# Kernel optimization log

Measured on AMD Instinct MI355X. Metric: run time of the kernel, lower is better.

The kernel has to match this reference:

```python
import jax, jax.numpy as jnp
import numpy as np

L1, L2, L3, L4 = 0.01, 0.001, 0.1, 100.0
DROP_P = 0.3

def setup_inputs() -> dict:
    key = jax.random.key(0)
    ks = jax.random.split(key, 6)
    n, p, h, c = 262144, 256, 256, 10
    x = jax.random.normal(ks[0], (n, p), dtype=jnp.float32)
    y = jax.random.randint(ks[1], (n,), 0, c, dtype=jnp.int64)
    drop_u = jax.random.uniform(ks[2], (n, h), dtype=jnp.float32)
    b1 = jax.random.normal(ks[3], (p, h), dtype=jnp.float32) / p
    b2 = jax.random.normal(ks[4], (h, c), dtype=jnp.float32) / h
    w = jax.random.normal(ks[5], (n, 1), dtype=jnp.float32) / n + 1.0 / np.sqrt(n).astype(np.float32)
    return {"x": x, "y": y, "drop_u": drop_u, "b1": b1, "b2": b2, "w": w}

def reference(x, y, drop_u, b1, b2, w):
    n, p = x.shape
    # MLP: ReLU -> Dropout(0.3) (inverted dropout, deterministic mask from drop_u)
    hdn = jax.nn.relu(x @ b1)
    keep = (drop_u > DROP_P).astype(x.dtype) / (1.0 - DROP_P)
    logits = (hdn * keep) @ b2  # [n, 10]
    pred = jnp.argmax(logits, axis=1)
    weight = w * w  # [n, 1]
    # per-sample CE; torch broadcast ce[n] * weight[n,1] -> [n,n], summed == ce.sum()*weight.sum()
    ce = -jnp.take_along_axis(jax.nn.log_softmax(logits, axis=-1), y[:, None], axis=1)[:, 0]
    loss = ce.sum() * weight.sum()
    # balancing regularizer: x.T @ diag(weight) @ x computed as column-scale-then-GEMM
    col = x.T @ weight  # [p, 1]
    gram = x.T @ (weight * x)  # [p, p] == x.T @ diag(weight) @ x
    bm = (gram - col @ col.T) * (1.0 - jnp.eye(p, dtype=x.dtype))
    loss = loss + L1 * (jnp.abs(b1).sum() + jnp.abs(b2).sum())
    loss = loss + L2 * jnp.sum(bm * bm)
    loss = loss + L3 * jnp.sum(weight * weight)
    loss = loss + L4 * (weight.sum() - 1.0) ** 2
    acc = jnp.mean((pred == y).astype(jnp.float32))
    return (loss, acc)
```

## Files before the change

### kernel.cpp

```cpp
#include <hip/hip_runtime.h>
#include <hip/hip_bf16.h>
#include <math.h>

typedef __bf16 v8bf  __attribute__((ext_vector_type(8)));
typedef __bf16 v4bf  __attribute__((ext_vector_type(4)));
typedef float  v16f  __attribute__((ext_vector_type(16)));
typedef float  v4f   __attribute__((ext_vector_type(4)));
typedef float  f4v   __attribute__((ext_vector_type(4)));

#define N_ROWS    262144
#define OFF_COL   64
#define OFF_GRAM  1024
#define OFF_WT    66560
#define B1T_BYTE  1314816
#define B2T_BYTE  1445888
#define ZERO_BYTES 266240

extern "C" __global__ __launch_bounds__(256) void prep_k(
    const float* __restrict__ w, const float* __restrict__ b1,
    const float* __restrict__ b2, float* __restrict__ wsf) {
  float* weight = wsf + OFF_WT;
  __bf16* b1T = (__bf16*)((char*)wsf + B1T_BYTE);
  __bf16* b2T = (__bf16*)((char*)wsf + B2T_BYTE);
  int gid = blockIdx.x * 256 + threadIdx.x;
  float wi = w[gid];
  float wt = wi * wi;
  weight[gid] = wt;
  float s1 = wt, s2 = wt * wt, a1 = 0.f, a2 = 0.f;
  if (gid < 65536) {
    int h = gid >> 8, p = gid & 255;
    float v = b1[p * 256 + h];
    b1T[gid] = (__bf16)v;
    a1 = fabsf(v);
  }
  if (gid < 4096) {
    int c = gid >> 8, h = gid & 255;
    float v = (c < 10) ? b2[h * 10 + c] : 0.f;
    b2T[gid] = (__bf16)v;
    a2 = fabsf(v);
  }
  #pragma unroll
  for (int off = 32; off > 0; off >>= 1) {
    s1 += __shfl_down(s1, off);
    s2 += __shfl_down(s2, off);
    a1 += __shfl_down(a1, off);
    a2 += __shfl_down(a2, off);
  }
  if ((threadIdx.x & 63) == 0) {
    atomicAdd(&wsf[1], s1);
    atomicAdd(&wsf[2], s2);
    if (blockIdx.x < 256) atomicAdd(&wsf[3], a1);
    if (blockIdx.x < 16)  atomicAdd(&wsf[4], a2);
  }
}

extern "C" __global__ __launch_bounds__(256, 2) void mlp_k(
    const float* __restrict__ x, const int* __restrict__ y,
    const float* __restrict__ du, float* __restrict__ wsf) {
  const __bf16* b1T = (const __bf16*)((const char*)wsf + B1T_BYTE);
  const __bf16* b2T = (const __bf16*)((const char*)wsf + B2T_BYTE);
  __shared__ union U {
    struct { __bf16 xs[128 * 40]; __bf16 b1s[256 * 40]; } m;
    struct { __bf16 hk[128 * 136]; float lg[128 * 16]; } l;
  } sm;
  const int tid = threadIdx.x;
  const int wv = tid >> 6, L = tid & 63;
  const int l32 = L & 31, lh = L >> 5;
  const int mb = 64 * (wv >> 1), nb = 128 * (wv & 1);
  const long rowBase = (long)blockIdx.x * 128;

  v16f acc[2][4] = {};

  for (int kc = 0; kc < 256; kc += 32) {
    __syncthreads();
    #pragma unroll
    for (int i = 0; i < 4; i++) {
      int f = tid + 256 * i;
      int r = f >> 3, c4 = f & 7;
      f4v v = ((const f4v*)x)[(rowBase + r) * 64 + (kc >> 2) + c4];
      v4bf o;
      o[0] = (__bf16)v[0]; o[1] = (__bf16)v[1]; o[2] = (__bf16)v[2]; o[3] = (__bf16)v[3];
      *(v4bf*)&sm.m.xs[r * 40 + 4 * c4] = o;
    }
    #pragma unroll
    for (int i = 0; i < 4; i++) {
      int f = tid + 256 * i;
      int nr = f >> 2, c = f & 3;
      *(v8bf*)&sm.m.b1s[nr * 40 + 8 * c] = *(const v8bf*)&b1T[nr * 256 + kc + 8 * c];
    }
    __syncthreads();
    #pragma unroll
    for (int ks = 0; ks < 32; ks += 16) {
      v8bf a0 = *(const v8bf*)&sm.m.xs[(mb + l32) * 40 + ks + 8 * lh];
      v8bf a1 = *(const v8bf*)&sm.m.xs[(mb + 32 + l32) * 40 + ks + 8 * lh];
      v8bf b[4];
      #pragma unroll
      for (int tn = 0; tn < 4; tn++)
        b[tn] = *(const v8bf*)&sm.m.b1s[(nb + 32 * tn + l32) * 40 + ks + 8 * lh];
      #pragma unroll
      for (int tn = 0; tn < 4; tn++) {
        acc[0][tn] = __builtin_amdgcn_mfma_f32_32x32x16_bf16(a0, b[tn], acc[0][tn], 0, 0, 0);
        acc[1][tn] = __builtin_amdgcn_mfma_f32_32x32x16_bf16(a1, b[tn], acc[1][tn], 0, 0, 0);
      }
    }
  }
  #pragma unroll
  for (int tm = 0; tm < 2; tm++)
    #pragma unroll
    for (int tn = 0; tn < 4; tn++)
      #pragma unroll
      for (int r = 0; r < 16; r++) {
        int row = mb + 32 * tm + (r & 3) + 8 * (r >> 2) + 4 * lh;
        int cg = nb + 32 * tn + l32;
        float u = du[(rowBase + row) * 256 + cg];
        float v = acc[tm][tn][r];
        v = fmaxf(v, 0.f);
        acc[tm][tn][r] = (u > 0.3f) ? v * (1.0f / 0.7f) : 0.f;
      }

  v4f lacc[2] = {};
  #pragma unroll
  for (int hc = 0; hc < 2; hc++) {
    __syncthreads();
    if ((wv & 1) == hc) {
      #pragma unroll
      for (int tm = 0; tm < 2; tm++)
        #pragma unroll
        for (int tn = 0; tn < 4; tn++)
          #pragma unroll
          for (int r = 0; r < 16; r++) {
            int row = mb + 32 * tm + (r & 3) + 8 * (r >> 2) + 4 * lh;
            int cl = 32 * tn + l32;
            sm.l.hk[row * 136 + cl] = (__bf16)acc[tm][tn][r];
          }
    }
    __syncthreads();
    #pragma unroll
    for (int i = 0; i < 2; i++) {
      int mt = 2 * wv + i;
      #pragma unroll
      for (int kk = 0; kk < 4; kk++) {
        v8bf a  = *(const v8bf*)&sm.l.hk[(16 * mt + (L & 15)) * 136 + 32 * kk + 8 * (L >> 4)];
        v8bf bb = *(const v8bf*)&b2T[(L & 15) * 256 + 128 * hc + 32 * kk + 8 * (L >> 4)];
        lacc[i] = __builtin_amdgcn_mfma_f32_16x16x32_bf16(a, bb, lacc[i], 0, 0, 0);
      }
    }
  }
  #pragma unroll
  for (int i = 0; i < 2; i++) {
    int mt = 2 * wv + i;
    #pragma unroll
    for (int r = 0; r < 4; r++)
      sm.l.lg[(16 * mt + 4 * (L >> 4) + r) * 16 + (L & 15)] = lacc[i][r];
  }
  __syncthreads();
  float ce = 0.f;
  int cor = 0;
  if (tid < 128) {
    const float* lr = &sm.l.lg[tid * 16];
    float mx = lr[0];
    int am = 0;
    #pragma unroll
    for (int c = 1; c < 10; c++)
      if (lr[c] > mx) { mx = lr[c]; am = c; }
    float s = 0.f;
    #pragma unroll
    for (int c = 0; c < 10; c++) s += expf(lr[c] - mx);
    int yt = y[rowBase + tid];
    ce = logf(s) + mx - lr[yt];
    cor = (am == yt) ? 1 : 0;
  }
  #pragma unroll
  for (int off = 32; off > 0; off >>= 1) ce += __shfl_down(ce, off);
  unsigned long long bal = __ballot(cor != 0);
  if (L == 0 && wv < 2) {
    atomicAdd(&wsf[0], ce);
    atomicAdd((int*)&wsf[8], (int)__popcll(bal));
  }
}

extern "C" __global__ __launch_bounds__(512, 1) void gram_k(
    const float* __restrict__ x, float* __restrict__ wsf) {
  const float* weight = wsf + OFF_WT;
  float* gram = wsf + OFF_GRAM;
  __shared__ __bf16 xT[256 * 40];
  __shared__ __bf16 wxT[256 * 40];
  const int tid = threadIdx.x;
  const int wv = tid >> 6, L = tid & 63;
  const int l32 = L & 31, lh = L >> 5;
  const int mb = 64 * (wv >> 1), nb = 128 * (wv & 1);
  const long base = (long)blockIdx.x * 1024;
  v16f acc[2][4] = {};
  float colAcc = 0.f;
  for (int ch = 0; ch < 32; ch++) {
    long k0 = base + ch * 32;
    __syncthreads();
    #pragma unroll
    for (int i = 0; i < 4; i++) {
      int f = tid + 512 * i;
      int k = f & 31, cg = f >> 5;
      f4v v = ((const f4v*)x)[(k0 + k) * 64 + cg];
      float wk = weight[k0 + k];
      #pragma unroll
      for (int d = 0; d < 4; d++) {
        int col = 4 * cg + d;
        xT[col * 40 + k]  = (__bf16)v[d];
        wxT[col * 40 + k] = (__bf16)(wk * v[d]);
      }
    }
    __syncthreads();
    if (tid < 256) {
      #pragma unroll
      for (int q = 0; q < 4; q++) {
        v8bf vv = *(const v8bf*)&wxT[tid * 40 + 8 * q];
        #pragma unroll
        for (int j = 0; j < 8; j++) colAcc += (float)vv[j];
      }
    }
    #pragma unroll
    for (int ks = 0; ks < 32; ks += 16) {
      v8bf a0 = *(const v8bf*)&xT[(mb + l32) * 40 + ks + 8 * lh];
      v8bf a1 = *(const v8bf*)&xT[(mb + 32 + l32) * 40 + ks + 8 * lh];
      v8bf b[4];
      #pragma unroll
      for (int tn = 0; tn < 4; tn++)
        b[tn] = *(const v8bf*)&wxT[(nb + 32 * tn + l32) * 40 + ks + 8 * lh];
      #pragma unroll
      for (int tn = 0; tn < 4; tn++) {
        acc[0][tn] = __builtin_amdgcn_mfma_f32_32x32x16_bf16(a0, b[tn], acc[0][tn], 0, 0, 0);
        acc[1][tn] = __builtin_amdgcn_mfma_f32_32x32x16_bf16(a1, b[tn], acc[1][tn], 0, 0, 0);
      }
    }
  }
  #pragma unroll
  for (int tm = 0; tm < 2; tm++)
    #pragma unroll
    for (int tn = 0; tn < 4; tn++)
      #pragma unroll
      for (int r = 0; r < 16; r++) {
        int row = mb + 32 * tm + (r & 3) + 8 * (r >> 2) + 4 * lh;
        int cg = nb + 32 * tn + l32;
        atomicAdd(&gram[row * 256 + cg], acc[tm][tn][r]);
      }
  if (tid < 256) atomicAdd(&wsf[OFF_COL + tid], colAcc);
}

extern "C" __global__ __launch_bounds__(256) void fin_k(
    const float* __restrict__ wsf, float* __restrict__ out) {
  __shared__ float colS[256];
  __shared__ float red[256];
  int t = threadIdx.x;
  colS[t] = wsf[OFF_COL + t];
  __syncthreads();
  const float* gram = wsf + OFF_GRAM;
  float ct = colS[t];
  float bm = 0.f;
  for (int j = 0; j < 256; j++) {
    float d = gram[t * 256 + j] - ct * colS[j];
    if (j != t) bm += d * d;
  }
  red[t] = bm;
  __syncthreads();
  for (int s = 128; s > 0; s >>= 1) {
    if (t < s) red[t] += red[t + s];
    __syncthreads();
  }
  if (t == 0) {
    float ce = wsf[0], wsum = wsf[1], w4 = wsf[2], ab1 = wsf[3], ab2 = wsf[4];
    int cor = *(const int*)&wsf[8];
    float loss = ce * wsum
               + 0.01f * (ab1 + ab2)
               + 0.001f * red[0]
               + 0.1f * w4
               + 100.f * (wsum - 1.f) * (wsum - 1.f);
    out[0] = loss;
    out[1] = (float)cor * (1.0f / 262144.0f);
  }
}

extern "C" void kernel_launch(void* const* d_in, const int* in_sizes, int n_in,
                              void* d_out, int out_size, void* d_ws, size_t ws_size,
                              hipStream_t stream) {
  const float* x  = (const float*)d_in[0];
  const int*   y  = (const int*)d_in[1];
  const float* du = (const float*)d_in[2];
  const float* b1 = (const float*)d_in[3];
  const float* b2 = (const float*)d_in[4];
  const float* w  = (const float*)d_in[5];
  float* wsf = (float*)d_ws;

  hipMemsetAsync(d_ws, 0, ZERO_BYTES, stream);
  prep_k<<<1024, 256, 0, stream>>>(w, b1, b2, wsf);
  mlp_k<<<2048, 256, 0, stream>>>(x, y, du, wsf);
  gram_k<<<256, 512, 0, stream>>>(x, wsf);
  fin_k<<<1, 256, 0, stream>>>(wsf, (float*)d_out);
}
```

Baseline: 860.3 us.

## Retile MLP and gram kernels, split gram atomics across copies, reorder launches

The MLP kernel now processes 64 rows per block with four waves each owning 64 hidden columns, which raises occupancy and removes the two-pass hidden-to-logit staging. The gram kernel loads x column-major with 64-row chunks, computes the weighted column sums in fp32, and spreads its atomics over four gram copies to cut contention. fin_k sums the four copies with 1024 threads, and gram_k now launches before mlp_k, possibly to reuse x in cache. This raises workspace memset size and changes the colsum precision.

```diff
diff --git a/kernel.cpp b/kernel.cpp
--- a/kernel.cpp
+++ b/kernel.cpp
@@ -8,13 +8,12 @@
 typedef float  v4f   __attribute__((ext_vector_type(4)));
 typedef float  f4v   __attribute__((ext_vector_type(4)));
 
-#define N_ROWS    262144
-#define OFF_COL   64
+#define OFF_COL   16
 #define OFF_GRAM  1024
-#define OFF_WT    66560
-#define B1T_BYTE  1314816
-#define B2T_BYTE  1445888
-#define ZERO_BYTES 266240
+#define OFF_WT    263168
+#define B1T_BYTE  2101248
+#define B2T_BYTE  2232320
+#define ZERO_BYTES 1052672
 
 extern "C" __global__ __launch_bounds__(256) void prep_k(
     const float* __restrict__ w, const float* __restrict__ b1,
@@ -54,27 +53,93 @@
   }
 }
 
-extern "C" __global__ __launch_bounds__(256, 2) void mlp_k(
+extern "C" __global__ __launch_bounds__(512, 2) void gram_k(
+    const float* __restrict__ x, float* __restrict__ wsf) {
+  const float* weight = wsf + OFF_WT;
+  float* gram = wsf + OFF_GRAM + (blockIdx.x & 3) * 65536;
+  __shared__ __bf16 xT[256 * 72];
+  __shared__ __bf16 wxT[256 * 72];
+  const int tid = threadIdx.x;
+  const int wv = tid >> 6, L = tid & 63;
+  const int l32 = L & 31, lh = L >> 5;
+  const int mb = 64 * (wv >> 1), nb = 128 * (wv & 1);
+  const int col = tid & 255, rh = tid >> 8;
+  const int base = blockIdx.x * 1024;
+  v16f acc[2][4] = {};
+  float colAcc = 0.f;
+
+  for (int ch = 0; ch < 16; ch++) {
+    int k0 = base + 64 * ch;
+    __syncthreads();
+    #pragma unroll
+    for (int s = 0; s < 8; s++) {
+      int krow = 32 * rh + 4 * s;
+      float v0 = x[(k0 + krow + 0) * 256 + col];
+      float v1 = x[(k0 + krow + 1) * 256 + col];
+      float v2 = x[(k0 + krow + 2) * 256 + col];
+      float v3 = x[(k0 + krow + 3) * 256 + col];
+      float w0 = weight[k0 + krow + 0];
+      float w1 = weight[k0 + krow + 1];
+      float w2 = weight[k0 + krow + 2];
+      float w3 = weight[k0 + krow + 3];
+      colAcc += w0 * v0 + w1 * v1 + w2 * v2 + w3 * v3;
+      v4bf xa, wa;
+      xa[0] = (__bf16)v0; xa[1] = (__bf16)v1; xa[2] = (__bf16)v2; xa[3] = (__bf16)v3;
+      wa[0] = (__bf16)(w0 * v0); wa[1] = (__bf16)(w1 * v1);
+      wa[2] = (__bf16)(w2 * v2); wa[3] = (__bf16)(w3 * v3);
+      *(v4bf*)&xT[col * 72 + krow]  = xa;
+      *(v4bf*)&wxT[col * 72 + krow] = wa;
+    }
+    __syncthreads();
+    #pragma unroll
+    for (int ks = 0; ks < 64; ks += 16) {
+      v8bf a0 = *(const v8bf*)&xT[(mb + l32) * 72 + ks + 8 * lh];
+      v8bf a1 = *(const v8bf*)&xT[(mb + 32 + l32) * 72 + ks + 8 * lh];
+      v8bf b[4];
+      #pragma unroll
+      for (int tn = 0; tn < 4; tn++)
+        b[tn] = *(const v8bf*)&wxT[(nb + 32 * tn + l32) * 72 + ks + 8 * lh];
+      #pragma unroll
+      for (int tn = 0; tn < 4; tn++) {
+        acc[0][tn] = __builtin_amdgcn_mfma_f32_32x32x16_bf16(a0, b[tn], acc[0][tn], 0, 0, 0);
+        acc[1][tn] = __builtin_amdgcn_mfma_f32_32x32x16_bf16(a1, b[tn], acc[1][tn], 0, 0, 0);
+      }
+    }
+  }
+  #pragma unroll
+  for (int tm = 0; tm < 2; tm++)
+    #pragma unroll
+    for (int tn = 0; tn < 4; tn++)
+      #pragma unroll
+      for (int r = 0; r < 16; r++) {
+        int row = mb + 32 * tm + (r & 3) + 8 * (r >> 2) + 4 * lh;
+        int cg = nb + 32 * tn + l32;
+        atomicAdd(&gram[row * 256 + cg], acc[tm][tn][r]);
+      }
+  atomicAdd(&wsf[OFF_COL + col], colAcc);
+}
+
+extern "C" __global__ __launch_bounds__(256, 4) void mlp_k(
     const float* __restrict__ x, const int* __restrict__ y,
     const float* __restrict__ du, float* __restrict__ wsf) {
   const __bf16* b1T = (const __bf16*)((const char*)wsf + B1T_BYTE);
   const __bf16* b2T = (const __bf16*)((const char*)wsf + B2T_BYTE);
   __shared__ union U {
-    struct { __bf16 xs[128 * 40]; __bf16 b1s[256 * 40]; } m;
-    struct { __bf16 hk[128 * 136]; float lg[128 * 16]; } l;
+    struct { __bf16 xs[64 * 40]; __bf16 b1s[256 * 40]; } m;
+    struct { __bf16 hk[64 * 264]; float lg[64 * 16]; } l;
   } sm;
   const int tid = threadIdx.x;
   const int wv = tid >> 6, L = tid & 63;
   const int l32 = L & 31, lh = L >> 5;
-  const int mb = 64 * (wv >> 1), nb = 128 * (wv & 1);
-  const long rowBase = (long)blockIdx.x * 128;
-
-  v16f acc[2][4] = {};
+  const int nb = 64 * wv;
+  const int rowBase = blockIdx.x * 64;
+
+  v16f acc[2][2] = {};
 
   for (int kc = 0; kc < 256; kc += 32) {
     __syncthreads();
     #pragma unroll
-    for (int i = 0; i < 4; i++) {
+    for (int i = 0; i < 2; i++) {
       int f = tid + 256 * i;
       int r = f >> 3, c4 = f & 7;
       f4v v = ((const f4v*)x)[(rowBase + r) * 64 + (kc >> 2) + c4];
@@ -91,26 +156,23 @@
     __syncthreads();
     #pragma unroll
     for (int ks = 0; ks < 32; ks += 16) {
-      v8bf a0 = *(const v8bf*)&sm.m.xs[(mb + l32) * 40 + ks + 8 * lh];
-      v8bf a1 = *(const v8bf*)&sm.m.xs[(mb + 32 + l32) * 40 + ks + 8 * lh];
-      v8bf b[4];
-      #pragma unroll
-      for (int tn = 0; tn < 4; tn++)
-        b[tn] = *(const v8bf*)&sm.m.b1s[(nb + 32 * tn + l32) * 40 + ks + 8 * lh];
-      #pragma unroll
-      for (int tn = 0; tn < 4; tn++) {
-        acc[0][tn] = __builtin_amdgcn_mfma_f32_32x32x16_bf16(a0, b[tn], acc[0][tn], 0, 0, 0);
-        acc[1][tn] = __builtin_amdgcn_mfma_f32_32x32x16_bf16(a1, b[tn], acc[1][tn], 0, 0, 0);
-      }
+      v8bf a0 = *(const v8bf*)&sm.m.xs[(l32) * 40 + ks + 8 * lh];
+      v8bf a1 = *(const v8bf*)&sm.m.xs[(32 + l32) * 40 + ks + 8 * lh];
+      v8bf b0 = *(const v8bf*)&sm.m.b1s[(nb + l32) * 40 + ks + 8 * lh];
+      v8bf b1f = *(const v8bf*)&sm.m.b1s[(nb + 32 + l32) * 40 + ks + 8 * lh];
+      acc[0][0] = __builtin_amdgcn_mfma_f32_32x32x16_bf16(a0, b0,  acc[0][0], 0, 0, 0);
+      acc[0][1] = __builtin_amdgcn_mfma_f32_32x32x16_bf16(a0, b1f, acc[0][1], 0, 0, 0);
+      acc[1][0] = __builtin_amdgcn_mfma_f32_32x32x16_bf16(a1, b0,  acc[1][0], 0, 0, 0);
+      acc[1][1] = __builtin_amdgcn_mfma_f32_32x32x16_bf16(a1, b1f, acc[1][1], 0, 0, 0);
     }
   }
   #pragma unroll
   for (int tm = 0; tm < 2; tm++)
     #pragma unroll
-    for (int tn = 0; tn < 4; tn++)
+    for (int tn = 0; tn < 2; tn++)
       #pragma unroll
       for (int r = 0; r < 16; r++) {
-        int row = mb + 32 * tm + (r & 3) + 8 * (r >> 2) + 4 * lh;
+        int row = 32 * tm + (r & 3) + 8 * (r >> 2) + 4 * lh;
         int cg = nb + 32 * tn + l32;
         float u = du[(rowBase + row) * 256 + cg];
         float v = acc[tm][tn][r];
@@ -118,45 +180,32 @@
         acc[tm][tn][r] = (u > 0.3f) ? v * (1.0f / 0.7f) : 0.f;
       }
 
-  v4f lacc[2] = {};
-  #pragma unroll
-  for (int hc = 0; hc < 2; hc++) {
-    __syncthreads();
-    if ((wv & 1) == hc) {
-      #pragma unroll
-      for (int tm = 0; tm < 2; tm++)
-        #pragma unroll
-        for (int tn = 0; tn < 4; tn++)
-          #pragma unroll
-          for (int r = 0; r < 16; r++) {
-            int row = mb + 32 * tm + (r & 3) + 8 * (r >> 2) + 4 * lh;
-            int cl = 32 * tn + l32;
-            sm.l.hk[row * 136 + cl] = (__bf16)acc[tm][tn][r];
-          }
-    }
-    __syncthreads();
-    #pragma unroll
-    for (int i = 0; i < 2; i++) {
-      int mt = 2 * wv + i;
-      #pragma unroll
-      for (int kk = 0; kk < 4; kk++) {
-        v8bf a  = *(const v8bf*)&sm.l.hk[(16 * mt + (L & 15)) * 136 + 32 * kk + 8 * (L >> 4)];
-        v8bf bb = *(const v8bf*)&b2T[(L & 15) * 256 + 128 * hc + 32 * kk + 8 * (L >> 4)];
-        lacc[i] = __builtin_amdgcn_mfma_f32_16x16x32_bf16(a, bb, lacc[i], 0, 0, 0);
-      }
-    }
-  }
-  #pragma unroll
-  for (int i = 0; i < 2; i++) {
-    int mt = 2 * wv + i;
-    #pragma unroll
-    for (int r = 0; r < 4; r++)
-      sm.l.lg[(16 * mt + 4 * (L >> 4) + r) * 16 + (L & 15)] = lacc[i][r];
-  }
+  __syncthreads();
+  #pragma unroll
+  for (int tm = 0; tm < 2; tm++)
+    #pragma unroll
+    for (int tn = 0; tn < 2; tn++)
+      #pragma unroll
+      for (int r = 0; r < 16; r++) {
+        int row = 32 * tm + (r & 3) + 8 * (r >> 2) + 4 * lh;
+        int cg = nb + 32 * tn + l32;
+        sm.l.hk[row * 264 + cg] = (__bf16)acc[tm][tn][r];
+      }
+  __syncthreads();
+  v4f lacc = {};
+  #pragma unroll
+  for (int kk = 0; kk < 8; kk++) {
+    v8bf a  = *(const v8bf*)&sm.l.hk[(16 * wv + (L & 15)) * 264 + 32 * kk + 8 * (L >> 4)];
+    v8bf bb = *(const v8bf*)&b2T[(L & 15) * 256 + 32 * kk + 8 * (L >> 4)];
+    lacc = __builtin_amdgcn_mfma_f32_16x16x32_bf16(a, bb, lacc, 0, 0, 0);
+  }
+  #pragma unroll
+  for (int r = 0; r < 4; r++)
+    sm.l.lg[(16 * wv + 4 * (L >> 4) + r) * 16 + (L & 15)] = lacc[r];
   __syncthreads();
   float ce = 0.f;
   int cor = 0;
-  if (tid < 128) {
+  if (tid < 64) {
     const float* lr = &sm.l.lg[tid * 16];
     float mx = lr[0];
     int am = 0;
@@ -170,102 +219,41 @@
     ce = logf(s) + mx - lr[yt];
     cor = (am == yt) ? 1 : 0;
   }
-  #pragma unroll
-  for (int off = 32; off > 0; off >>= 1) ce += __shfl_down(ce, off);
-  unsigned long long bal = __ballot(cor != 0);
-  if (L == 0 && wv < 2) {
-    atomicAdd(&wsf[0], ce);
-    atomicAdd((int*)&wsf[8], (int)__popcll(bal));
-  }
-}
-
-extern "C" __global__ __launch_bounds__(512, 1) void gram_k(
-    const float* __restrict__ x, float* __restrict__ wsf) {
-  const float* weight = wsf + OFF_WT;
-  float* gram = wsf + OFF_GRAM;
-  __shared__ __bf16 xT[256 * 40];
-  __shared__ __bf16 wxT[256 * 40];
-  const int tid = threadIdx.x;
-  const int wv = tid >> 6, L = tid & 63;
-  const int l32 = L & 31, lh = L >> 5;
-  const int mb = 64 * (wv >> 1), nb = 128 * (wv & 1);
-  const long base = (long)blockIdx.x * 1024;
-  v16f acc[2][4] = {};
-  float colAcc = 0.f;
-  for (int ch = 0; ch < 32; ch++) {
-    long k0 = base + ch * 32;
-    __syncthreads();
-    #pragma unroll
-    for (int i = 0; i < 4; i++) {
-      int f = tid + 512 * i;
-      int k = f & 31, cg = f >> 5;
-      f4v v = ((const f4v*)x)[(k0 + k) * 64 + cg];
-      float wk = weight[k0 + k];
-      #pragma unroll
-      for (int d = 0; d < 4; d++) {
-        int col = 4 * cg + d;
-        xT[col * 40 + k]  = (__bf16)v[d];
-        wxT[col * 40 + k] = (__bf16)(wk * v[d]);
-      }
-    }
-    __syncthreads();
-    if (tid < 256) {
-      #pragma unroll
-      for (int q = 0; q < 4; q++) {
-        v8bf vv = *(const v8bf*)&wxT[tid * 40 + 8 * q];
-        #pragma unroll
-        for (int j = 0; j < 8; j++) colAcc += (float)vv[j];
-      }
-    }
-    #pragma unroll
-    for (int ks = 0; ks < 32; ks += 16) {
-      v8bf a0 = *(const v8bf*)&xT[(mb + l32) * 40 + ks + 8 * lh];
-      v8bf a1 = *(const v8bf*)&xT[(mb + 32 + l32) * 40 + ks + 8 * lh];
-      v8bf b[4];
-      #pragma unroll
-      for (int tn = 0; tn < 4; tn++)
-        b[tn] = *(const v8bf*)&wxT[(nb + 32 * tn + l32) * 40 + ks + 8 * lh];
-      #pragma unroll
-      for (int tn = 0; tn < 4; tn++) {
-        acc[0][tn] = __builtin_amdgcn_mfma_f32_32x32x16_bf16(a0, b[tn], acc[0][tn], 0, 0, 0);
-        acc[1][tn] = __builtin_amdgcn_mfma_f32_32x32x16_bf16(a1, b[tn], acc[1][tn], 0, 0, 0);
-      }
-    }
-  }
-  #pragma unroll
-  for (int tm = 0; tm < 2; tm++)
-    #pragma unroll
-    for (int tn = 0; tn < 4; tn++)
-      #pragma unroll
-      for (int r = 0; r < 16; r++) {
-        int row = mb + 32 * tm + (r & 3) + 8 * (r >> 2) + 4 * lh;
-        int cg = nb + 32 * tn + l32;
-        atomicAdd(&gram[row * 256 + cg], acc[tm][tn][r]);
-      }
-  if (tid < 256) atomicAdd(&wsf[OFF_COL + tid], colAcc);
-}
-
-extern "C" __global__ __launch_bounds__(256) void fin_k(
+  if (wv == 0) {
+    #pragma unroll
+    for (int off = 32; off > 0; off >>= 1) ce += __shfl_down(ce, off);
+    unsigned long long bal = __ballot(cor != 0);
+    if (L == 0) {
+      atomicAdd(&wsf[0], ce);
+      atomicAdd((int*)&wsf[8], (int)__popcll(bal));
+    }
+  }
+}
+
+extern "C" __global__ __launch_bounds__(1024) void fin_k(
     const float* __restrict__ wsf, float* __restrict__ out) {
   __shared__ float colS[256];
-  __shared__ float red[256];
-  int t = threadIdx.x;
-  colS[t] = wsf[OFF_COL + t];
-  __syncthreads();
-  const float* gram = wsf + OFF_GRAM;
+  __shared__ float red[1024];
+  int tid = threadIdx.x;
+  if (tid < 256) colS[tid] = wsf[OFF_COL + tid];
+  __syncthreads();
+  int t = tid & 255, q = tid >> 8;
+  const float* g = wsf + OFF_GRAM;
   float ct = colS[t];
   float bm = 0.f;
-  for (int j = 0; j < 256; j++) {
-    float d = gram[t * 256 + j] - ct * colS[j];
-    if (j != t) bm += d * d;
-  }
-  red[t] = bm;
-  __syncthreads();
-  for (int s = 128; s > 0; s >>= 1) {
-    if (t < s) red[t] += red[t + s];
-    __syncthreads();
-  }
-  if (t == 0) {
+  for (int j = 64 * q; j < 64 * q + 64; j++) {
+    float gv = g[j * 256 + t] + g[65536 + j * 256 + t]
+             + g[131072 + j * 256 + t] + g[196608 + j * 256 + t];
+    float d = gv - colS[j] * ct;
+    bm += (j != t) ? d * d : 0.f;
+  }
+  red[tid] = bm;
+  __syncthreads();
+  for (int s = 512; s > 0; s >>= 1) {
+    if (tid < s) red[tid] += red[tid + s];
+    __syncthreads();
+  }
+  if (tid == 0) {
     float ce = wsf[0], wsum = wsf[1], w4 = wsf[2], ab1 = wsf[3], ab2 = wsf[4];
     int cor = *(const int*)&wsf[8];
     float loss = ce * wsum
@@ -291,7 +279,7 @@
 
   hipMemsetAsync(d_ws, 0, ZERO_BYTES, stream);
   prep_k<<<1024, 256, 0, stream>>>(w, b1, b2, wsf);
-  mlp_k<<<2048, 256, 0, stream>>>(x, y, du, wsf);
   gram_k<<<256, 512, 0, stream>>>(x, wsf);
-  fin_k<<<1, 256, 0, stream>>>(wsf, (float*)d_out);
-}
+  mlp_k<<<4096, 256, 0, stream>>>(x, y, du, wsf);
+  fin_k<<<1, 1024, 0, stream>>>(wsf, (float*)d_out);
+}
```

Result: faster. 818.0 us (-4.9%).
